# Kernel optimization log

Hardware: AMD Instinct MI355X
Metric: run time of the kernel (lower is better)

## Reference

```python
import jax, jax.numpy as jnp
import numpy as np

D_MODEL = 1024
NUM_EXPERTS = 8
TOP_K = 2


def setup_inputs() -> dict:
    key = jax.random.key(0)
    ks = jax.random.split(key, 8)
    d, e = D_MODEL, NUM_EXPERTS
    s = 0.02
    return {
        "x": jax.random.normal(ks[0], (2, 2048, d), dtype=jnp.float32),
        "router_w": jax.random.normal(ks[1], (d, e), dtype=jnp.float32) * s,
        "router_b": jnp.zeros((e,), dtype=jnp.float32),
        "w1": jax.random.normal(ks[2], (e, d, 4 * d), dtype=jnp.float32) * s,
        "b1": jnp.zeros((e, 4 * d), dtype=jnp.float32),
        "w2": jax.random.normal(ks[3], (e, 4 * d, d), dtype=jnp.float32) * s,
        "b2": jnp.zeros((e, d), dtype=jnp.float32),
    }


def reference(x, router_w, router_b, w1, b1, w2, b2):
    orig_shape = x.shape
    d = x.shape[-1]
    xf = x.reshape(-1, d)                      # [T, d]
    T = xf.shape[0]

    logits = xf @ router_w + router_b          # [T, E]
    probs = jax.nn.softmax(logits, axis=-1)    # [T, E]
    top_v, top_i = jax.lax.top_k(probs, TOP_K)  # [T, k]
    top_v = top_v / jnp.sum(top_v, axis=-1, keepdims=True)

    # dense combine weights, zero except the top-k experts per token
    comb = jnp.zeros_like(probs).at[jnp.arange(T)[:, None], top_i].add(top_v)  # [T, E]

    # run every expert on every token (dense grouped GEMM), then weighted combine
    h = jax.nn.gelu(jnp.einsum("td,edf->etf", xf, w1) + b1[:, None, :], approximate=False)  # [E, T, 4d]
    y = jnp.einsum("etf,efd->etd", h, w2) + b2[:, None, :]                                   # [E, T, d]
    out = jnp.einsum("te,etd->td", comb, y)                                                   # [T, d]

    mean_probs = probs.mean(axis=0)
    aux_loss = jnp.var(mean_probs, ddof=1)     # torch.var default is unbiased
    return out.reshape(orig_shape), aux_loss
```

## Files before the change

### kernel.cpp

```cpp
#include <hip/hip_runtime.h>


#define TOKENS 4096
#define DMODEL 1024
#define NEXP   8
#define DFF    4096
#define NROWS  (2*TOKENS)

typedef __bf16 bf16_t;
typedef __bf16 bf16x8 __attribute__((ext_vector_type(8)));
typedef __bf16 bf16x4 __attribute__((ext_vector_type(4)));
typedef float  f32x4  __attribute__((ext_vector_type(4)));

__device__ __forceinline__ void gl_lds16(const void* g, void* l) {
    __builtin_amdgcn_global_load_lds(
        (const __attribute__((address_space(1))) void*)g,
        (__attribute__((address_space(3))) void*)l, 16, 0, 0);
}

__global__ __launch_bounds__(64) void router_k(
    const float* __restrict__ x, const float* __restrict__ rw,
    const float* __restrict__ rb, int* __restrict__ cnt,
    int* __restrict__ tok_e, int* __restrict__ tok_pos,
    float* __restrict__ tok_w, float* __restrict__ probs)
{
    int t = blockIdx.x;
    int lane = threadIdx.x;
    const float* xr = x + (size_t)t * DMODEL;
    float s[NEXP];
#pragma unroll
    for (int e = 0; e < NEXP; e++) s[e] = 0.f;
    for (int i = lane; i < DMODEL; i += 64) {
        float xv = xr[i];
        const float* wr = rw + (size_t)i * NEXP;
#pragma unroll
        for (int e = 0; e < NEXP; e++) s[e] += xv * wr[e];
    }
#pragma unroll
    for (int e = 0; e < NEXP; e++) {
#pragma unroll
        for (int o = 32; o > 0; o >>= 1) s[e] += __shfl_down(s[e], o, 64);
    }
    if (lane == 0) {
        float mx = -1e30f;
#pragma unroll
        for (int e = 0; e < NEXP; e++) { s[e] += rb[e]; mx = fmaxf(mx, s[e]); }
        float den = 0.f;
#pragma unroll
        for (int e = 0; e < NEXP; e++) { s[e] = expf(s[e] - mx); den += s[e]; }
        float inv = 1.f / den;
#pragma unroll
        for (int e = 0; e < NEXP; e++) { s[e] *= inv; probs[t * NEXP + e] = s[e]; }
        int e0 = 0;
#pragma unroll
        for (int e = 1; e < NEXP; e++) if (s[e] > s[e0]) e0 = e;
        int e1 = (e0 == 0) ? 1 : 0;
#pragma unroll
        for (int e = 0; e < NEXP; e++) if (e != e0 && s[e] > s[e1]) e1 = e;
        float sw = s[e0] + s[e1];
        int p0 = atomicAdd(&cnt[e0], 1);
        int p1 = atomicAdd(&cnt[e1], 1);
        tok_e[2 * t] = e0;       tok_e[2 * t + 1] = e1;
        tok_pos[2 * t] = p0;     tok_pos[2 * t + 1] = p1;
        tok_w[2 * t] = s[e0] / sw; tok_w[2 * t + 1] = s[e1] / sw;
    }
}

__global__ void offsets_k(const int* __restrict__ cnt, int* __restrict__ off)
{
    if (threadIdx.x == 0) {
        int a = 0;
        for (int e = 0; e < NEXP; e++) { off[e] = a; a += cnt[e]; }
        off[NEXP] = a;
    }
}

__global__ void scatter_k(const int* __restrict__ tok_e, const int* __restrict__ tok_pos,
                          const float* __restrict__ tok_w, const int* __restrict__ off,
                          int* __restrict__ rows_tok, float* __restrict__ roww)
{
    int i = blockIdx.x * blockDim.x + threadIdx.x;
    if (i < 2 * TOKENS) {
        int e = tok_e[i];
        int g = off[e] + tok_pos[i];
        rows_tok[g] = i >> 1;
        roww[g] = tok_w[i];
    }
}

__global__ __launch_bounds__(256) void convx_k(const float4* __restrict__ in,
                                               bf16x4* __restrict__ o, int n4)
{
    int i = blockIdx.x * blockDim.x + threadIdx.x;
    if (i < n4) {
        float4 v = in[i];
        bf16x4 r = { (bf16_t)v.x, (bf16_t)v.y, (bf16_t)v.z, (bf16_t)v.w };
        o[i] = r;
    }
}

__global__ __launch_bounds__(256) void transconv_k(const float* __restrict__ in,
                                                   bf16_t* __restrict__ o, int K, int N)
{
    __shared__ float tile[32][33];
    int e = blockIdx.z;
    int n0 = blockIdx.x * 32, k0 = blockIdx.y * 32;
    int tx = threadIdx.x & 31, ty = threadIdx.x >> 5;
    const float* src = in + ((size_t)e * K + k0) * N + n0;
#pragma unroll
    for (int r = 0; r < 32; r += 8) tile[ty + r][tx] = src[(size_t)(ty + r) * N + tx];
    __syncthreads();
    bf16_t* dst = o + ((size_t)e * N + n0) * K + k0;
#pragma unroll
    for (int r = 0; r < 32; r += 8) dst[(size_t)(ty + r) * K + tx] = (bf16_t)tile[tx][ty + r];
}

template<int KDIM, int MODE>
__global__ __launch_bounds__(256, 2) void ffn_gemm_k(
    const bf16_t* __restrict__ A, const bf16_t* __restrict__ Bt,
    const float* __restrict__ bias,
    const int* __restrict__ cnt, const int* __restrict__ off,
    const int* __restrict__ rows_tok, const float* __restrict__ roww,
    bf16_t* __restrict__ hbuf, float* __restrict__ out, int N)
{
    int e = blockIdx.z;
    int M = cnt[e];
    int m0 = blockIdx.y * 128;
    if (m0 >= M) return;
    int n0 = blockIdx.x * 128;
    int base = off[e];

    __shared__ __align__(16) bf16_t lA[128 * 64];
    __shared__ __align__(16) bf16_t lB[128 * 64];

    int tid = threadIdx.x;
    int wave = tid >> 6;
    int lane = tid & 63;
    int sc = (lane & 7) ^ (lane >> 3);

    const bf16_t* aRow[4];
    const bf16_t* bRow[4];
#pragma unroll
    for (int i = 0; i < 4; i++) {
        int r = (wave * 4 + i) * 8 + (lane >> 3);
        int gr = m0 + r; if (gr > M - 1) gr = M - 1;
        if (MODE == 0) {
            int tok = rows_tok[base + gr];
            aRow[i] = A + (size_t)tok * KDIM;
        } else {
            aRow[i] = A + (size_t)(base + gr) * KDIM;
        }
        bRow[i] = Bt + ((size_t)e * N + n0 + r) * KDIM;
    }

    f32x4 acc[4][4];
    f32x4 zero = { 0.f, 0.f, 0.f, 0.f };
#pragma unroll
    for (int i = 0; i < 4; i++)
#pragma unroll
        for (int j = 0; j < 4; j++) acc[i][j] = zero;

    int wrow = wave >> 1, wcol = wave & 1;

#pragma unroll 1
    for (int kk = 0; kk < KDIM / 64; ++kk) {
        int koff = kk * 64 + sc * 8;
#pragma unroll
        for (int i = 0; i < 4; i++) {
            gl_lds16(aRow[i] + koff, &lA[(wave * 4 + i) * 512]);
            gl_lds16(bRow[i] + koff, &lB[(wave * 4 + i) * 512]);
        }
        __syncthreads();
#pragma unroll
        for (int ks = 0; ks < 2; ++ks) {
            bf16x8 af[4], bfr[4];
#pragma unroll
            for (int mt = 0; mt < 4; mt++) {
                int r = wrow * 64 + mt * 16 + (lane & 15);
                int ch = (ks * 4 + (lane >> 4)) ^ (r & 7);
                af[mt] = *(const bf16x8*)&lA[r * 64 + ch * 8];
            }
#pragma unroll
            for (int nt = 0; nt < 4; nt++) {
                int c = wcol * 64 + nt * 16 + (lane & 15);
                int ch = (ks * 4 + (lane >> 4)) ^ (c & 7);
                bfr[nt] = *(const bf16x8*)&lB[c * 64 + ch * 8];
            }
#pragma unroll
            for (int mt = 0; mt < 4; mt++)
#pragma unroll
                for (int nt = 0; nt < 4; nt++)
                    acc[mt][nt] = __builtin_amdgcn_mfma_f32_16x16x32_bf16(
                        af[mt], bfr[nt], acc[mt][nt], 0, 0, 0);
        }
        __syncthreads();
    }

    float bv[4];
#pragma unroll
    for (int nt = 0; nt < 4; nt++)
        bv[nt] = bias[(size_t)e * N + n0 + wcol * 64 + nt * 16 + (lane & 15)];

#pragma unroll
    for (int mt = 0; mt < 4; mt++) {
#pragma unroll
        for (int q = 0; q < 4; q++) {
            int r = wrow * 64 + mt * 16 + (lane >> 4) * 4 + q;
            int gm = m0 + r;
            if (gm < M) {
                if (MODE == 0) {
                    size_t hrow = (size_t)(base + gm) * DFF;
#pragma unroll
                    for (int nt = 0; nt < 4; nt++) {
                        float v = acc[mt][nt][q] + bv[nt];
                        v = 0.5f * v * (1.f + erff(v * 0.70710678118654752f));
                        int c = n0 + wcol * 64 + nt * 16 + (lane & 15);
                        hbuf[hrow + c] = (bf16_t)v;
                    }
                } else {
                    int g = base + gm;
                    int tok = rows_tok[g];
                    float wgt = roww[g];
                    size_t orow = (size_t)tok * DMODEL;
#pragma unroll
                    for (int nt = 0; nt < 4; nt++) {
                        float v = acc[mt][nt][q] + bv[nt];
                        int c = n0 + wcol * 64 + nt * 16 + (lane & 15);
                        atomicAdd(&out[orow + c], wgt * v);
                    }
                }
            }
        }
    }
}

__global__ __launch_bounds__(256) void aux_k(const float* __restrict__ probs,
                                             float* __restrict__ out_aux)
{
    __shared__ float red[256];
    __shared__ float mexp[NEXP];
    float s[NEXP];
#pragma unroll
    for (int e = 0; e < NEXP; e++) s[e] = 0.f;
    for (int t = threadIdx.x; t < TOKENS; t += 256) {
#pragma unroll
        for (int e = 0; e < NEXP; e++) s[e] += probs[t * NEXP + e];
    }
    for (int e = 0; e < NEXP; e++) {
        red[threadIdx.x] = s[e];
        __syncthreads();
        for (int st = 128; st > 0; st >>= 1) {
            if (threadIdx.x < st) red[threadIdx.x] += red[threadIdx.x + st];
            __syncthreads();
        }
        if (threadIdx.x == 0) mexp[e] = red[0] / (float)TOKENS;
        __syncthreads();
    }
    if (threadIdx.x == 0) {
        float mean = 0.f;
        for (int e = 0; e < NEXP; e++) mean += mexp[e];
        mean /= (float)NEXP;
        float v = 0.f;
        for (int e = 0; e < NEXP; e++) { float d = mexp[e] - mean; v += d * d; }
        out_aux[0] = v / (float)(NEXP - 1);
    }
}

extern "C" void kernel_launch(void* const* d_in, const int* in_sizes, int n_in,
                              void* d_out, int out_size, void* d_ws, size_t ws_size,
                              hipStream_t stream)
{
    const float* x  = (const float*)d_in[0];
    const float* rw = (const float*)d_in[1];
    const float* rb = (const float*)d_in[2];
    const float* w1 = (const float*)d_in[3];
    const float* b1 = (const float*)d_in[4];
    const float* w2 = (const float*)d_in[5];
    const float* b2 = (const float*)d_in[6];
    float* out = (float*)d_out;

    char* p = (char*)d_ws;
    auto alloc = [&](size_t b) { char* q = p; p += (b + 255) & ~(size_t)255; return q; };
    int*    cnt      = (int*)   alloc(NEXP * sizeof(int));
    int*    off      = (int*)   alloc((NEXP + 1) * sizeof(int));
    int*    tok_e    = (int*)   alloc(2 * TOKENS * sizeof(int));
    int*    tok_pos  = (int*)   alloc(2 * TOKENS * sizeof(int));
    float*  tok_w    = (float*) alloc(2 * TOKENS * sizeof(float));
    int*    rows_tok = (int*)   alloc(NROWS * sizeof(int));
    float*  roww     = (float*) alloc(NROWS * sizeof(float));
    float*  probs    = (float*) alloc((size_t)TOKENS * NEXP * sizeof(float));
    bf16_t* xb       = (bf16_t*)alloc((size_t)TOKENS * DMODEL * 2);
    bf16_t* w1t      = (bf16_t*)alloc((size_t)NEXP * DFF * DMODEL * 2);
    bf16_t* w2t      = (bf16_t*)alloc((size_t)NEXP * DMODEL * DFF * 2);
    bf16_t* hbuf     = (bf16_t*)alloc((size_t)NROWS * DFF * 2);

    hipMemsetAsync(cnt, 0, NEXP * sizeof(int), stream);
    hipMemsetAsync(d_out, 0, (size_t)out_size * sizeof(float), stream);

    router_k<<<TOKENS, 64, 0, stream>>>(x, rw, rb, cnt, tok_e, tok_pos, tok_w, probs);
    offsets_k<<<1, 64, 0, stream>>>(cnt, off);
    scatter_k<<<(2 * TOKENS + 255) / 256, 256, 0, stream>>>(tok_e, tok_pos, tok_w, off,
                                                            rows_tok, roww);
    convx_k<<<(TOKENS * DMODEL / 4 + 255) / 256, 256, 0, stream>>>(
        (const float4*)x, (bf16x4*)xb, TOKENS * DMODEL / 4);
    transconv_k<<<dim3(DFF / 32, DMODEL / 32, NEXP), 256, 0, stream>>>(w1, w1t, DMODEL, DFF);
    transconv_k<<<dim3(DMODEL / 32, DFF / 32, NEXP), 256, 0, stream>>>(w2, w2t, DFF, DMODEL);

    ffn_gemm_k<DMODEL, 0><<<dim3(DFF / 128, TOKENS / 128, NEXP), 256, 0, stream>>>(
        xb, w1t, b1, cnt, off, rows_tok, roww, hbuf, out, DFF);
    ffn_gemm_k<DFF, 1><<<dim3(DMODEL / 128, TOKENS / 128, NEXP), 256, 0, stream>>>(
        hbuf, w2t, b2, cnt, off, rows_tok, roww, hbuf, out, DMODEL);

    aux_k<<<1, 256, 0, stream>>>(probs, out + (size_t)TOKENS * DMODEL);
}
```

Baseline: 707.2 us.

## Fuse x bf16 conversion into router, widen transpose tiles, remap GEMM grid

```diff
diff --git a/kernel.cpp b/kernel.cpp
--- a/kernel.cpp
+++ b/kernel.cpp
@@ -9,7 +9,6 @@
 
 typedef __bf16 bf16_t;
 typedef __bf16 bf16x8 __attribute__((ext_vector_type(8)));
-typedef __bf16 bf16x4 __attribute__((ext_vector_type(4)));
 typedef float  f32x4  __attribute__((ext_vector_type(4)));
 
 __device__ __forceinline__ void gl_lds16(const void* g, void* l) {
@@ -22,16 +21,19 @@
     const float* __restrict__ x, const float* __restrict__ rw,
     const float* __restrict__ rb, int* __restrict__ cnt,
     int* __restrict__ tok_e, int* __restrict__ tok_pos,
-    float* __restrict__ tok_w, float* __restrict__ probs)
+    float* __restrict__ tok_w, float* __restrict__ probs,
+    bf16_t* __restrict__ xb)
 {
     int t = blockIdx.x;
     int lane = threadIdx.x;
     const float* xr = x + (size_t)t * DMODEL;
+    bf16_t* xbr = xb + (size_t)t * DMODEL;
     float s[NEXP];
 #pragma unroll
     for (int e = 0; e < NEXP; e++) s[e] = 0.f;
     for (int i = lane; i < DMODEL; i += 64) {
         float xv = xr[i];
+        xbr[i] = (bf16_t)xv;
         const float* wr = rw + (size_t)i * NEXP;
 #pragma unroll
         for (int e = 0; e < NEXP; e++) s[e] += xv * wr[e];
@@ -88,46 +90,53 @@
     }
 }
 
-__global__ __launch_bounds__(256) void convx_k(const float4* __restrict__ in,
-                                               bf16x4* __restrict__ o, int n4)
-{
-    int i = blockIdx.x * blockDim.x + threadIdx.x;
-    if (i < n4) {
-        float4 v = in[i];
-        bf16x4 r = { (bf16_t)v.x, (bf16_t)v.y, (bf16_t)v.z, (bf16_t)v.w };
-        o[i] = r;
-    }
-}
-
+#define TP 65
 __global__ __launch_bounds__(256) void transconv_k(const float* __restrict__ in,
                                                    bf16_t* __restrict__ o, int K, int N)
 {
-    __shared__ float tile[32][33];
+    __shared__ float t[64 * TP];
     int e = blockIdx.z;
-    int n0 = blockIdx.x * 32, k0 = blockIdx.y * 32;
-    int tx = threadIdx.x & 31, ty = threadIdx.x >> 5;
+    int n0 = blockIdx.x * 64, k0 = blockIdx.y * 64;
+    int tid = threadIdx.x;
+    int c4 = tid & 15, r = tid >> 4;
     const float* src = in + ((size_t)e * K + k0) * N + n0;
 #pragma unroll
-    for (int r = 0; r < 32; r += 8) tile[ty + r][tx] = src[(size_t)(ty + r) * N + tx];
+    for (int p = 0; p < 4; p++) {
+        int k = r + p * 16;
+        float4 v = *(const float4*)(src + (size_t)k * N + c4 * 4);
+        float* d = &t[k * TP + c4 * 4];
+        d[0] = v.x; d[1] = v.y; d[2] = v.z; d[3] = v.w;
+    }
     __syncthreads();
+    int k8 = tid & 7, n = tid >> 3;
     bf16_t* dst = o + ((size_t)e * N + n0) * K + k0;
 #pragma unroll
-    for (int r = 0; r < 32; r += 8) dst[(size_t)(ty + r) * K + tx] = (bf16_t)tile[tx][ty + r];
-}
-
-template<int KDIM, int MODE>
-__global__ __launch_bounds__(256, 2) void ffn_gemm_k(
+    for (int p = 0; p < 2; p++) {
+        int nn = n + p * 32;
+        bf16x8 w;
+#pragma unroll
+        for (int j = 0; j < 8; j++) w[j] = (bf16_t)t[(k8 * 8 + j) * TP + nn];
+        *(bf16x8*)(dst + (size_t)nn * K + k8 * 8) = w;
+    }
+}
+
+template<int KDIM, int NT, int MODE>
+__global__ __launch_bounds__(256) void ffn_gemm_k(
     const bf16_t* __restrict__ A, const bf16_t* __restrict__ Bt,
     const float* __restrict__ bias,
     const int* __restrict__ cnt, const int* __restrict__ off,
     const int* __restrict__ rows_tok, const float* __restrict__ roww,
     bf16_t* __restrict__ hbuf, float* __restrict__ out, int N)
 {
-    int e = blockIdx.z;
+    int bid = blockIdx.x;
+    int e = bid & 7;
+    int rest = bid >> 3;
+    int yt = rest & 31;
+    int xt = rest >> 5;
     int M = cnt[e];
-    int m0 = blockIdx.y * 128;
+    int m0 = yt * 128;
     if (m0 >= M) return;
-    int n0 = blockIdx.x * 128;
+    int n0 = xt * 128;
     int base = off[e];
 
     __shared__ __align__(16) bf16_t lA[128 * 64];
@@ -297,18 +306,16 @@
     hipMemsetAsync(cnt, 0, NEXP * sizeof(int), stream);
     hipMemsetAsync(d_out, 0, (size_t)out_size * sizeof(float), stream);
 
-    router_k<<<TOKENS, 64, 0, stream>>>(x, rw, rb, cnt, tok_e, tok_pos, tok_w, probs);
+    router_k<<<TOKENS, 64, 0, stream>>>(x, rw, rb, cnt, tok_e, tok_pos, tok_w, probs, xb);
     offsets_k<<<1, 64, 0, stream>>>(cnt, off);
     scatter_k<<<(2 * TOKENS + 255) / 256, 256, 0, stream>>>(tok_e, tok_pos, tok_w, off,
                                                             rows_tok, roww);
-    convx_k<<<(TOKENS * DMODEL / 4 + 255) / 256, 256, 0, stream>>>(
-        (const float4*)x, (bf16x4*)xb, TOKENS * DMODEL / 4);
-    transconv_k<<<dim3(DFF / 32, DMODEL / 32, NEXP), 256, 0, stream>>>(w1, w1t, DMODEL, DFF);
-    transconv_k<<<dim3(DMODEL / 32, DFF / 32, NEXP), 256, 0, stream>>>(w2, w2t, DFF, DMODEL);
-
-    ffn_gemm_k<DMODEL, 0><<<dim3(DFF / 128, TOKENS / 128, NEXP), 256, 0, stream>>>(
+    transconv_k<<<dim3(DFF / 64, DMODEL / 64, NEXP), 256, 0, stream>>>(w1, w1t, DMODEL, DFF);
+    transconv_k<<<dim3(DMODEL / 64, DFF / 64, NEXP), 256, 0, stream>>>(w2, w2t, DFF, DMODEL);
+
+    ffn_gemm_k<DMODEL, 32, 0><<<NEXP * 32 * 32, 256, 0, stream>>>(
         xb, w1t, b1, cnt, off, rows_tok, roww, hbuf, out, DFF);
-    ffn_gemm_k<DFF, 1><<<dim3(DMODEL / 128, TOKENS / 128, NEXP), 256, 0, stream>>>(
+    ffn_gemm_k<DFF, 8, 1><<<NEXP * 32 * 8, 256, 0, stream>>>(
         hbuf, w2t, b2, cnt, off, rows_tok, roww, hbuf, out, DMODEL);
 
     aux_k<<<1, 256, 0, stream>>>(probs, out + (size_t)TOKENS * DMODEL);
```

Result: slower. 815.9 us (+15.4%).
